# Kernel optimization log

Hardware: AMD Instinct MI355X
Metric: run time of the kernel (lower is better)

Reference implementation:

```python
import jax, jax.numpy as jnp
import numpy as np
from jax import lax

B, N, M = 2, 16384, 4096
C1, C2 = 128, 256
H1, H2 = 256, 128  # mlp = [C1+C2, 256, 128]


def setup_inputs() -> dict:
    key = jax.random.key(0)
    ks = jax.random.split(key, 8)
    return {
        "unknown": jax.random.normal(ks[0], (B, N, 3), jnp.float32),
        "known": jax.random.normal(ks[1], (B, M, 3), jnp.float32),
        "unknow_feats": jax.random.normal(ks[2], (B, C1, N), jnp.float32),
        "known_feats": jax.random.normal(ks[3], (B, C2, M), jnp.float32),
        "W1": jax.random.normal(ks[4], (H1, C1 + C2), jnp.float32) * 0.05,
        "b1": jnp.zeros((H1,), jnp.float32),
        "W2": jax.random.normal(ks[5], (H2, H1), jnp.float32) * 0.05,
        "b2": jnp.zeros((H2,), jnp.float32),
    }


def reference(unknown, known, unknow_feats, known_feats, W1, b1, W2, b2):
    # Pairwise squared distances (B, n, m) via ||a||^2 + ||b||^2 - 2 a.b
    d2 = (
        jnp.sum(unknown * unknown, -1)[:, :, None]
        + jnp.sum(known * known, -1)[:, None, :]
        - 2.0 * jnp.einsum("bnd,bmd->bnm", unknown, known)
    )
    # 3 nearest neighbors
    neg_d2, idx = lax.top_k(-d2, 3)  # (B, n, 3)
    dist = jnp.sqrt(jnp.maximum(-neg_d2, 0.0))  # pointops returns sqrt distances
    dist_recip = 1.0 / (dist + 1e-8)
    weight = dist_recip / jnp.sum(dist_recip, axis=2, keepdims=True)  # (B, n, 3)
    # Gather neighbor features (B, C2, n, 3) and inverse-distance weighted sum
    gathered = jax.vmap(lambda f, i: f[:, i])(known_feats, idx)
    interpolated = jnp.sum(gathered * weight[:, None, :, :], axis=-1)  # (B, C2, n)
    new_features = jnp.concatenate([interpolated, unknow_feats], axis=1)  # (B, C1+C2, n)
    # Shared MLP (1x1 convs, bn=False -> conv bias + ReLU)
    h = jax.nn.relu(jnp.einsum("oc,bcn->bon", W1, new_features) + b1[None, :, None])
    out = jax.nn.relu(jnp.einsum("oc,bcn->bon", W2, h) + b2[None, :, None])
    return out  # (B, mlp[-1], n)
```

## Files before the change

kernel.cpp:

```cpp
#include <hip/hip_runtime.h>
#include <hip/hip_bf16.h>

#define BB 2
#define NN 16384
#define MM 4096
#define C1 128
#define C2 256
#define CIN 384
#define H1 256
#define H2 128
#define PT 32

typedef __attribute__((ext_vector_type(8))) short bf16x8;
typedef __attribute__((ext_vector_type(4))) float f32x4;

__device__ __forceinline__ short f32_to_bf16(float x) {
    unsigned u = __float_as_uint(x);
    u += 0x7fffu + ((u >> 16) & 1u);
    return (short)(u >> 16);
}
__device__ __forceinline__ unsigned pack_bf16x2(float a, float b) {
    __hip_bfloat162 h = __float22bfloat162_rn(make_float2(a, b));
    union { __hip_bfloat162 h; unsigned u; } cv;
    cv.h = h;
    return cv.u;
}

__global__ __launch_bounds__(256) void prep_kernel(
    const float* __restrict__ W1, const float* __restrict__ W2,
    const float* __restrict__ known,
    short* __restrict__ W1b, short* __restrict__ W2b,
    float4* __restrict__ kpk)
{
    int i = blockIdx.x * 256 + threadIdx.x;
    if (i < H1 * CIN) W1b[i] = f32_to_bf16(W1[i]);
    if (i < H2 * H1)  W2b[i] = f32_to_bf16(W2[i]);
    if (i < BB * MM) {
        float x = known[3 * i + 0], y = known[3 * i + 1], z = known[3 * i + 2];
        kpk[i] = make_float4(x, y, z, fmaf(x, x, fmaf(y, y, z * z)));
    }
}

__global__ __launch_bounds__(512) void knn3_kernel(
    const float* __restrict__ unknown,
    const float4* __restrict__ kpk,
    int*   __restrict__ idx_out,
    float* __restrict__ w_out)
{
    __shared__ float pd[8][64][3];
    __shared__ int   pi[8][64][3];

    const int b    = blockIdx.y;
    const int tid  = threadIdx.x;
    const int lane = tid & 63;
    const int wv   = __builtin_amdgcn_readfirstlane(tid >> 6);
    const int n    = blockIdx.x * 64 + lane;

    const float ux = unknown[((size_t)b * NN + n) * 3 + 0];
    const float uy = unknown[((size_t)b * NN + n) * 3 + 1];
    const float uz = unknown[((size_t)b * NN + n) * 3 + 2];
    const float ax = -2.f * ux, ay = -2.f * uy, az = -2.f * uz;
    const float un = fmaf(ux, ux, fmaf(uy, uy, uz * uz));

    const int mbase = wv * (MM / 8);
    const float4* __restrict__ kp = kpk + (size_t)b * MM + mbase;

    float v0 = 3e38f, v1 = 3e38f, v2 = 3e38f;
    int   j0 = 0,     j1 = 0,     j2 = 0;
    for (int m = 0; m < MM / 8; m += 8) {
        #pragma unroll
        for (int u = 0; u < 8; ++u) {
            const float4 k = kp[m + u];
            float sc = fmaf(ax, k.x, fmaf(ay, k.y, fmaf(az, k.z, k.w)));
            const int mm = mbase + m + u;
            const bool lt0 = sc < v0;
            const bool lt1 = sc < v1;
            const bool lt2 = sc < v2;
            v2 = __builtin_amdgcn_fmed3f(v1, sc, v2);
            j2 = lt1 ? j1 : (lt2 ? mm : j2);
            v1 = __builtin_amdgcn_fmed3f(v0, sc, v1);
            j1 = lt0 ? j0 : (lt1 ? mm : j1);
            v0 = fminf(sc, v0);
            j0 = lt0 ? mm : j0;
        }
    }
    pd[wv][lane][0] = v0; pd[wv][lane][1] = v1; pd[wv][lane][2] = v2;
    pi[wv][lane][0] = j0; pi[wv][lane][1] = j1; pi[wv][lane][2] = j2;
    __syncthreads();

    if (tid < 64) {
        float r0 = 3e38f, r1 = 3e38f, r2 = 3e38f;
        int   q0 = 0,     q1 = 0,     q2 = 0;
        #pragma unroll
        for (int ww = 0; ww < 8; ++ww) {
            #pragma unroll
            for (int k = 0; k < 3; ++k) {
                float d = pd[ww][lane][k];
                int   j = pi[ww][lane][k];
                const bool lt0 = d < r0;
                const bool lt1 = d < r1;
                const bool lt2 = d < r2;
                r2 = __builtin_amdgcn_fmed3f(r1, d, r2);
                q2 = lt1 ? q1 : (lt2 ? j : q2);
                r1 = __builtin_amdgcn_fmed3f(r0, d, r1);
                q1 = lt0 ? q0 : (lt1 ? j : q1);
                r0 = fminf(d, r0);
                q0 = lt0 ? j : q0;
            }
        }
        float d0 = sqrtf(fmaxf(r0 + un, 0.f));
        float d1 = sqrtf(fmaxf(r1 + un, 0.f));
        float d2 = sqrtf(fmaxf(r2 + un, 0.f));
        float i0 = 1.f / (d0 + 1e-8f);
        float i1 = 1.f / (d1 + 1e-8f);
        float i2 = 1.f / (d2 + 1e-8f);
        float s  = i0 + i1 + i2;
        const size_t ob = ((size_t)b * NN + n) * 3;
        idx_out[ob + 0] = q0; idx_out[ob + 1] = q1; idx_out[ob + 2] = q2;
        w_out[ob + 0] = i0 / s; w_out[ob + 1] = i1 / s; w_out[ob + 2] = i2 / s;
    }
}

__global__ __launch_bounds__(256) void transpose_kernel(
    const float* __restrict__ KF, float* __restrict__ KT)
{
    __shared__ float tl[32][33];
    const int b  = blockIdx.z;
    const int m0 = blockIdx.x * 32;
    const int c0 = blockIdx.y * 32;
    const int tx = threadIdx.x & 31;
    const int ty = threadIdx.x >> 5;
    #pragma unroll
    for (int r = 0; r < 4; ++r) {
        int c = ty + r * 8;
        tl[c][tx] = KF[((size_t)b * C2 + c0 + c) * MM + m0 + tx];
    }
    __syncthreads();
    #pragma unroll
    for (int r = 0; r < 4; ++r) {
        int m = ty + r * 8;
        KT[((size_t)b * MM + m0 + m) * C2 + c0 + tx] = tl[tx][m];
    }
}

__global__ __launch_bounds__(256, 3) void fp_mlp_mfma_kernel(
    const float* __restrict__ unknow_feats,
    const float* __restrict__ KT,
    const short* __restrict__ W1b,
    const float* __restrict__ b1,
    const short* __restrict__ W2b,
    const float* __restrict__ b2,
    const int*   __restrict__ idx,
    const float* __restrict__ wgt,
    float* __restrict__ out)
{
    #define XROW 392
    #define HROW 264
    __shared__ short Xs[PT][XROW];
    __shared__ short Hs[PT][HROW];
    __shared__ int   Is[PT * 3];
    __shared__ float Ws[PT * 3];

    const int tid  = threadIdx.x;
    const int blocks_per_b = NN / PT;
    const int b    = blockIdx.x / blocks_per_b;
    const int n0   = (blockIdx.x % blocks_per_b) * PT;
    const int w    = tid >> 6;
    const int lane = tid & 63;
    const int lr   = lane & 15;
    const int lq   = lane >> 4;

    if (tid < PT * 3) {
        const size_t base = ((size_t)b * NN + n0) * 3;
        Is[tid] = idx[base + tid];
        Ws[tid] = wgt[base + tid];
    }
    __syncthreads();

    {
        const float* KTb = KT + (size_t)b * MM * C2;
        const int c4 = (lane << 2);
        #pragma unroll
        for (int pp = 0; pp < PT; pp += 4) {
            const int p = pp + w;
            const int   i0 = Is[3 * p + 0], i1 = Is[3 * p + 1], i2 = Is[3 * p + 2];
            const float w0 = Ws[3 * p + 0], w1 = Ws[3 * p + 1], w2 = Ws[3 * p + 2];
            const float4 A = *(const float4*)(KTb + (size_t)i0 * C2 + c4);
            const float4 Bv = *(const float4*)(KTb + (size_t)i1 * C2 + c4);
            const float4 Cv = *(const float4*)(KTb + (size_t)i2 * C2 + c4);
            float vx = fmaf(w0, A.x, fmaf(w1, Bv.x, w2 * Cv.x));
            float vy = fmaf(w0, A.y, fmaf(w1, Bv.y, w2 * Cv.y));
            float vz = fmaf(w0, A.z, fmaf(w1, Bv.z, w2 * Cv.z));
            float vw = fmaf(w0, A.w, fmaf(w1, Bv.w, w2 * Cv.w));
            uint2 pk;
            pk.x = pack_bf16x2(vx, vy);
            pk.y = pack_bf16x2(vz, vw);
            *(uint2*)&Xs[p][c4] = pk;
        }
        const float* UFb = unknow_feats + (size_t)b * C1 * NN + n0;
        #pragma unroll
        for (int i = 0; i < 4; ++i) {
            int e  = i * 256 + tid;
            int cc = e >> 3;
            int nq = (e & 7) << 2;
            const float4 f = *(const float4*)(UFb + (size_t)cc * NN + nq);
            Xs[nq + 0][C2 + cc] = f32_to_bf16(f.x);
            Xs[nq + 1][C2 + cc] = f32_to_bf16(f.y);
            Xs[nq + 2][C2 + cc] = f32_to_bf16(f.z);
            Xs[nq + 3][C2 + cc] = f32_to_bf16(f.w);
        }
    }
    __syncthreads();

    {
        f32x4 acc[4][2];
        #pragma unroll
        for (int t = 0; t < 4; ++t)
            #pragma unroll
            for (int p = 0; p < 2; ++p) acc[t][p] = (f32x4){0.f, 0.f, 0.f, 0.f};

        for (int k0 = 0; k0 < CIN; k0 += 32) {
            bf16x8 a[4], x[2];
            #pragma unroll
            for (int t = 0; t < 4; ++t)
                a[t] = *(const bf16x8*)(W1b + (size_t)(w * 64 + t * 16 + lr) * CIN + k0 + lq * 8);
            #pragma unroll
            for (int p = 0; p < 2; ++p)
                x[p] = *(bf16x8*)&Xs[p * 16 + lr][k0 + lq * 8];
            #pragma unroll
            for (int t = 0; t < 4; ++t)
                #pragma unroll
                for (int p = 0; p < 2; ++p)
                    acc[t][p] = __builtin_amdgcn_mfma_f32_16x16x32_bf16(a[t], x[p], acc[t][p], 0, 0, 0);
        }
        #pragma unroll
        for (int t = 0; t < 4; ++t) {
            const int obase = w * 64 + t * 16 + lq * 4;
            float bb0 = b1[obase + 0], bb1 = b1[obase + 1],
                  bb2 = b1[obase + 2], bb3 = b1[obase + 3];
            #pragma unroll
            for (int p = 0; p < 2; ++p) {
                uint2 pk;
                pk.x = pack_bf16x2(fmaxf(acc[t][p].x + bb0, 0.f),
                                   fmaxf(acc[t][p].y + bb1, 0.f));
                pk.y = pack_bf16x2(fmaxf(acc[t][p].z + bb2, 0.f),
                                   fmaxf(acc[t][p].w + bb3, 0.f));
                *(uint2*)&Hs[p * 16 + lr][obase] = pk;
            }
        }
    }
    __syncthreads();

    {
        f32x4 acc[2][2];
        #pragma unroll
        for (int t = 0; t < 2; ++t)
            #pragma unroll
            for (int p = 0; p < 2; ++p) acc[t][p] = (f32x4){0.f, 0.f, 0.f, 0.f};

        for (int k0 = 0; k0 < H1; k0 += 32) {
            bf16x8 a[2], h[2];
            #pragma unroll
            for (int t = 0; t < 2; ++t)
                a[t] = *(const bf16x8*)(W2b + (size_t)(w * 32 + t * 16 + lr) * H1 + k0 + lq * 8);
            #pragma unroll
            for (int p = 0; p < 2; ++p)
                h[p] = *(bf16x8*)&Hs[p * 16 + lr][k0 + lq * 8];
            #pragma unroll
            for (int t = 0; t < 2; ++t)
                #pragma unroll
                for (int p = 0; p < 2; ++p)
                    acc[t][p] = __builtin_amdgcn_mfma_f32_16x16x32_bf16(a[t], h[p], acc[t][p], 0, 0, 0);
        }
        #pragma unroll
        for (int t = 0; t < 2; ++t) {
            const int obase = w * 32 + t * 16 + lq * 4;
            #pragma unroll
            for (int p = 0; p < 2; ++p) {
                const int n = n0 + p * 16 + lr;
                #pragma unroll
                for (int r = 0; r < 4; ++r) {
                    const int o = obase + r;
                    out[((size_t)b * H2 + o) * NN + n] =
                        fmaxf(((const float*)&acc[t][p])[r] + b2[o], 0.f);
                }
            }
        }
    }
    #undef XROW
    #undef HROW
}

extern "C" void kernel_launch(void* const* d_in, const int* in_sizes, int n_in,
                              void* d_out, int out_size, void* d_ws, size_t ws_size,
                              hipStream_t stream) {
    const float* unknown      = (const float*)d_in[0];
    const float* known        = (const float*)d_in[1];
    const float* unknow_feats = (const float*)d_in[2];
    const float* known_feats  = (const float*)d_in[3];
    const float* W1           = (const float*)d_in[4];
    const float* b1           = (const float*)d_in[5];
    const float* W2           = (const float*)d_in[6];
    const float* b2           = (const float*)d_in[7];
    float* out = (float*)d_out;

    char* ws = (char*)d_ws;
    int*    idx = (int*)(ws);
    float*  wgt = (float*)(ws + 393216);
    short*  W1b = (short*)(ws + 786432);
    short*  W2b = (short*)(ws + 983040);
    float4* kpk = (float4*)(ws + 1048576);
    float*  KT  = (float*)(ws + 1179648);

    prep_kernel<<<(H1 * CIN + 255) / 256, 256, 0, stream>>>(W1, W2, known, W1b, W2b, kpk);

    dim3 gK(NN / 64, BB);
    knn3_kernel<<<gK, 512, 0, stream>>>(unknown, kpk, idx, wgt);

    dim3 gT(MM / 32, C2 / 32, BB);
    transpose_kernel<<<gT, 256, 0, stream>>>(known_feats, KT);

    fp_mlp_mfma_kernel<<<BB * (NN / PT), 256, 0, stream>>>(
        unknow_feats, KT, W1b, b1, W2b, b2, idx, wgt, out);
}
```

Measured before the change: 195.5 us.

## Split KNN into value-only top-3 pass and index recovery rescan

Result: faster. 187.1 us (-4.3%).

```diff
diff --git a/kernel.cpp b/kernel.cpp
--- a/kernel.cpp
+++ b/kernel.cpp
@@ -41,14 +41,17 @@
     }
 }
 
-__global__ __launch_bounds__(512) void knn3_kernel(
+__global__ __launch_bounds__(1024) void knn3_kernel(
     const float* __restrict__ unknown,
     const float4* __restrict__ kpk,
     int*   __restrict__ idx_out,
     float* __restrict__ w_out)
 {
-    __shared__ float pd[8][64][3];
-    __shared__ int   pi[8][64][3];
+    __shared__ float pdv[16][64][3];
+    __shared__ float vf[64];
+    __shared__ float msc[64][8];
+    __shared__ int   mid[64][8];
+    __shared__ int   cnt[64];
 
     const int b    = blockIdx.y;
     const int tid  = threadIdx.x;
@@ -56,57 +59,79 @@
     const int wv   = __builtin_amdgcn_readfirstlane(tid >> 6);
     const int n    = blockIdx.x * 64 + lane;
 
+    if (tid < 64) cnt[tid] = 0;
+
     const float ux = unknown[((size_t)b * NN + n) * 3 + 0];
     const float uy = unknown[((size_t)b * NN + n) * 3 + 1];
     const float uz = unknown[((size_t)b * NN + n) * 3 + 2];
     const float ax = -2.f * ux, ay = -2.f * uy, az = -2.f * uz;
     const float un = fmaf(ux, ux, fmaf(uy, uy, uz * uz));
 
-    const int mbase = wv * (MM / 8);
+    const int mbase = wv * 256;
     const float4* __restrict__ kp = kpk + (size_t)b * MM + mbase;
 
     float v0 = 3e38f, v1 = 3e38f, v2 = 3e38f;
-    int   j0 = 0,     j1 = 0,     j2 = 0;
-    for (int m = 0; m < MM / 8; m += 8) {
+    for (int m = 0; m < 256; m += 8) {
         #pragma unroll
         for (int u = 0; u < 8; ++u) {
             const float4 k = kp[m + u];
             float sc = fmaf(ax, k.x, fmaf(ay, k.y, fmaf(az, k.z, k.w)));
-            const int mm = mbase + m + u;
-            const bool lt0 = sc < v0;
-            const bool lt1 = sc < v1;
-            const bool lt2 = sc < v2;
             v2 = __builtin_amdgcn_fmed3f(v1, sc, v2);
-            j2 = lt1 ? j1 : (lt2 ? mm : j2);
             v1 = __builtin_amdgcn_fmed3f(v0, sc, v1);
-            j1 = lt0 ? j0 : (lt1 ? mm : j1);
             v0 = fminf(sc, v0);
-            j0 = lt0 ? mm : j0;
-        }
-    }
-    pd[wv][lane][0] = v0; pd[wv][lane][1] = v1; pd[wv][lane][2] = v2;
-    pi[wv][lane][0] = j0; pi[wv][lane][1] = j1; pi[wv][lane][2] = j2;
+        }
+    }
+    pdv[wv][lane][0] = v0; pdv[wv][lane][1] = v1; pdv[wv][lane][2] = v2;
     __syncthreads();
 
     if (tid < 64) {
         float r0 = 3e38f, r1 = 3e38f, r2 = 3e38f;
-        int   q0 = 0,     q1 = 0,     q2 = 0;
-        #pragma unroll
-        for (int ww = 0; ww < 8; ++ww) {
+        #pragma unroll
+        for (int ww = 0; ww < 16; ++ww) {
             #pragma unroll
             for (int k = 0; k < 3; ++k) {
-                float d = pd[ww][lane][k];
-                int   j = pi[ww][lane][k];
-                const bool lt0 = d < r0;
-                const bool lt1 = d < r1;
-                const bool lt2 = d < r2;
+                float d = pdv[ww][tid][k];
                 r2 = __builtin_amdgcn_fmed3f(r1, d, r2);
-                q2 = lt1 ? q1 : (lt2 ? j : q2);
                 r1 = __builtin_amdgcn_fmed3f(r0, d, r1);
-                q1 = lt0 ? q0 : (lt1 ? j : q1);
                 r0 = fminf(d, r0);
-                q0 = lt0 ? j : q0;
             }
+        }
+        vf[tid] = r2;
+    }
+    __syncthreads();
+
+    const float v2f = vf[lane];
+    for (int m = 0; m < 256; m += 8) {
+        #pragma unroll
+        for (int u = 0; u < 8; ++u) {
+            const float4 k = kp[m + u];
+            float sc = fmaf(ax, k.x, fmaf(ay, k.y, fmaf(az, k.z, k.w)));
+            if (sc <= v2f) {
+                int c = atomicAdd(&cnt[lane], 1);
+                if (c < 8) { msc[lane][c] = sc; mid[lane][c] = mbase + m + u; }
+            }
+        }
+    }
+    __syncthreads();
+
+    if (tid < 64) {
+        const int c = cnt[tid] < 8 ? cnt[tid] : 8;
+        float r0 = 3e38f, r1 = 3e38f, r2 = 3e38f;
+        int   q0 = 0x7FFFFFFF, q1 = 0x7FFFFFFF, q2 = 0x7FFFFFFF;
+        #pragma unroll
+        for (int k = 0; k < 8; ++k) {
+            float d = (k < c) ? msc[tid][k] : 3e38f;
+            int   j = (k < c) ? mid[tid][k] : 0x7FFFFFFF;
+            const bool lt0 = (d < r0) || (d == r0 && j < q0);
+            const bool lt1 = (d < r1) || (d == r1 && j < q1);
+            const bool lt2 = (d < r2) || (d == r2 && j < q2);
+            float nr2 = lt1 ? r1 : (lt2 ? d : r2);
+            int   nq2 = lt1 ? q1 : (lt2 ? j : q2);
+            float nr1 = lt0 ? r0 : (lt1 ? d : r1);
+            int   nq1 = lt0 ? q0 : (lt1 ? j : q1);
+            float nr0 = lt0 ? d : r0;
+            int   nq0 = lt0 ? j : q0;
+            r0 = nr0; r1 = nr1; r2 = nr2; q0 = nq0; q1 = nq1; q2 = nq2;
         }
         float d0 = sqrtf(fmaxf(r0 + un, 0.f));
         float d1 = sqrtf(fmaxf(r1 + un, 0.f));
@@ -315,7 +340,7 @@
     prep_kernel<<<(H1 * CIN + 255) / 256, 256, 0, stream>>>(W1, W2, known, W1b, W2b, kpk);
 
     dim3 gK(NN / 64, BB);
-    knn3_kernel<<<gK, 512, 0, stream>>>(unknown, kpk, idx, wgt);
+    knn3_kernel<<<gK, 1024, 0, stream>>>(unknown, kpk, idx, wgt);
 
     dim3 gT(MM / 32, C2 / 32, BB);
     transpose_kernel<<<gT, 256, 0, stream>>>(known_feats, KT);
```
